# Optimization experiments

Measured on AMD Instinct MI355X. Metric: run time of the kernel, lower is better.

The kernel has to match this reference:

```python
import jax, jax.numpy as jnp
import numpy as np

N_NODES = 100000
N_EDGES = 1600000
F_IN, F_HID, F_OUT = 128, 128, 16
NEG_SLOPE = 0.2


def _glorot(key, shape):
    fan = sum(shape)
    return jax.random.uniform(key, shape, jnp.float32, -1.0, 1.0) * jnp.sqrt(6.0 / fan)


def setup_inputs() -> dict:
    key = jax.random.key(0)
    ks = jax.random.split(key, 16)
    x = jax.random.normal(ks[0], (N_NODES, F_IN), jnp.float32)
    edge_index = jax.random.randint(ks[1], (2, N_EDGES), 0, N_NODES, jnp.int64)
    d1, d2, d3 = F_HID, F_HID // 2, F_OUT
    return {
        'x': x,
        'edge_index': edge_index,
        'W1': _glorot(ks[2], (F_IN, d1)), 'a_src1': _glorot(ks[3], (d1,)), 'a_dst1': _glorot(ks[4], (d1,)), 'b1': jnp.zeros((d1,), jnp.float32),
        'W2': _glorot(ks[5], (d1, d2)), 'a_src2': _glorot(ks[6], (d2,)), 'a_dst2': _glorot(ks[7], (d2,)), 'b2': jnp.zeros((d2,), jnp.float32),
        'W3': _glorot(ks[8], (d2, d3)), 'a_src3': _glorot(ks[9], (d3,)), 'a_dst3': _glorot(ks[10], (d3,)), 'b3': jnp.zeros((d3,), jnp.float32),
    }


def gat_conv(x, src, dst, W, a_s, a_d, b):
    # x: [N, Fin] -> h: [N, Fout]; src/dst: [E] (self-loops included)
    h = x @ W
    e = jax.nn.leaky_relu(h @ a_s, NEG_SLOPE * 0 + NEG_SLOPE)  # placeholder avoided below
    # attention logits per edge: leaky_relu(alpha_src[src] + alpha_dst[dst])
    al_s = h @ a_s  # [N]
    al_d = h @ a_d  # [N]
    logits = jax.nn.leaky_relu(al_s[src] + al_d[dst], NEG_SLOPE)  # [E]
    # numerically stable softmax over incoming edges of each dst node
    m = jax.ops.segment_max(logits, dst, num_segments=N_NODES)
    m = jnp.where(jnp.isfinite(m), m, 0.0)
    ex = jnp.exp(logits - m[dst])
    denom = jax.ops.segment_sum(ex, dst, num_segments=N_NODES)
    alpha = ex / denom[dst]  # self-loops guarantee denom > 0
    out = jax.ops.segment_sum(alpha[:, None] * h[src], dst, num_segments=N_NODES)
    return out + b


def reference(x, edge_index, W1, a_src1, a_dst1, b1, W2, a_src2, a_dst2, b2, W3, a_src3, a_dst3, b3):
    loops = jnp.arange(N_NODES, dtype=edge_index.dtype)
    src = jnp.concatenate([edge_index[0], loops])
    dst = jnp.concatenate([edge_index[1], loops])
    h = gat_conv(x, src, dst, W1, a_src1, a_dst1, b1)
    h = jax.nn.relu(h)  # dropout p=0.5 is identity in eval mode
    h = gat_conv(h, src, dst, W2, a_src2, a_dst2, b2)
    h = jax.nn.relu(h)
    out = gat_conv(h, src, dst, W3, a_src3, a_dst3, b3)
    return out
```

## Files before the change

kernel.cpp:

```cpp
#include <hip/hip_runtime.h>
#include <hip/hip_bf16.h>

typedef __hip_bfloat16 bf16;
typedef __attribute__((ext_vector_type(8))) __bf16 bf16x8;
typedef __attribute__((ext_vector_type(4))) float f32x4;

static constexpr int N = 100000;
static constexpr int E = 1600000;
static constexpr int ETOT = E + N;
static constexpr float SLOPE = 0.2f;

__device__ __constant__ int c_poff[12] = {0, 16384, 16512, 16640,
                                          16768, 24960, 25024, 25088,
                                          25152, 26176, 26192, 26208};
static constexpr int PTOT = 26224;
static constexpr int H_POFF[12] = {0, 16384, 16512, 16640, 16768, 24960,
                                   25024, 25088, 25152, 26176, 26192, 26208};

struct Src12 { const void* p[12]; };

__device__ __forceinline__ float bfLo(unsigned u) { return __uint_as_float(u << 16); }
__device__ __forceinline__ float bfHi(unsigned u) { return __uint_as_float(u & 0xFFFF0000u); }

__device__ __forceinline__ void fma8(const uint4 r, float e, float* acc) {
  acc[0] = fmaf(e, bfLo(r.x), acc[0]);
  acc[1] = fmaf(e, bfHi(r.x), acc[1]);
  acc[2] = fmaf(e, bfLo(r.y), acc[2]);
  acc[3] = fmaf(e, bfHi(r.y), acc[3]);
  acc[4] = fmaf(e, bfLo(r.z), acc[4]);
  acc[5] = fmaf(e, bfHi(r.z), acc[5]);
  acc[6] = fmaf(e, bfLo(r.w), acc[6]);
  acc[7] = fmaf(e, bfHi(r.w), acc[7]);
}

__device__ __forceinline__ float edge_ex(float l) {
  l = (l > 0.f) ? l : SLOPE * l;
  return __expf(l);
}

__device__ __forceinline__ void loadEdge(const int* __restrict__ ei32,
                                         const long long* __restrict__ ei64,
                                         int use64, int t, int& s, int& d) {
  if (t >= E) { s = d = t - E; return; }
  if (use64) { s = (int)ei64[t]; d = (int)ei64[E + t]; }
  else       { s = ei32[t];      d = ei32[E + t]; }
}

__device__ __forceinline__ unsigned pk2(float a, float b) {
  bf16 x = __float2bfloat16(a), y = __float2bfloat16(b);
  unsigned short ux = *(unsigned short*)&x, uy = *(unsigned short*)&y;
  return ((unsigned)uy << 16) | ux;
}

static constexpr int CHUNK = 8192;
static constexpr int NCHK  = (ETOT + CHUNK - 1) / CHUNK;
static constexpr int NB1   = (N + 511) / 512;
static constexpr int M1    = NB1 * NCHK;
static constexpr int SBLK  = (M1 + 255) / 256;

__global__ __launch_bounds__(256) void detect_kernel(
    const unsigned long long* __restrict__ ei64,
    const unsigned short* __restrict__ w1u16, int* __restrict__ flags) {
  const int t = threadIdx.x;
  __shared__ unsigned long long bl[4];
  __shared__ unsigned long long sb64;
  const int w = t >> 6;
  bool p64 = (t < 64) && (ei64[t] >= (unsigned long long)N);
  unsigned long long b64 = __ballot(p64);
  if (t == 0) sb64 = b64;
  bool pf = (((w1u16[t] >> 7) & 0xFFu) >= 126u);
  unsigned long long bf_ = __ballot(pf);
  if ((t & 63) == 0) bl[w] = bf_;
  __syncthreads();
  if (t == 0) {
    flags[0] = (sb64 == 0ull) ? 1 : 0;
    flags[1] = ((bl[0] | bl[1] | bl[2] | bl[3]) != 0ull) ? 1 : 0;
  }
}

static constexpr int PB_PAR = (PTOT + 255) / 256;
static constexpr int PB_W1  = 128 * 128 / 256;
static constexpr int PB_W2  = 128 * 64 / 256;
static constexpr int PB_W3  = 64 * 16 / 256;
static constexpr int PB_TOT = NCHK + PB_PAR + PB_W1 + PB_W2 + PB_W3;

__device__ __forceinline__ void conv_w(const void* W, int kd, int dout, int f32,
                                       bf16* __restrict__ wt, int idx) {
  int n = idx / kd, k = idx - n * kd;
  float v = f32 ? ((const float*)W)[k * dout + n]
                : __bfloat162float(((const bf16*)W)[k * dout + n]);
  wt[idx] = __float2bfloat16(v);
}

__global__ __launch_bounds__(256) void prep_kernel(
    const int* __restrict__ ei32, const long long* __restrict__ ei64,
    const int* __restrict__ flags, int* __restrict__ c1,
    Src12 s, float* __restrict__ prm,
    bf16* __restrict__ w1t, bf16* __restrict__ w2t, bf16* __restrict__ w3t) {
  const int b = blockIdx.x, tid = threadIdx.x;
  const int f64 = flags[0], f32 = flags[1];
  if (b < NCHK) {
    __shared__ int h1[NB1];
    if (tid < NB1) h1[tid] = 0;
    __syncthreads();
    const int t0 = b * CHUNK;
#pragma unroll 4
    for (int i = tid; i < CHUNK; i += 256) {
      int t = t0 + i;
      if (t < ETOT) {
        int d = (t >= E) ? (t - E) : (f64 ? (int)ei64[E + t] : ei32[E + t]);
        atomicAdd(&h1[d >> 9], 1);
      }
    }
    __syncthreads();
    if (tid < NB1) c1[tid * NCHK + b] = h1[tid];
  } else if (b < NCHK + PB_PAR) {
    int t = (b - NCHK) * 256 + tid;
    if (t < PTOT) {
      int k = 0;
#pragma unroll
      for (int i = 1; i < 12; ++i)
        if (t >= c_poff[i]) k = i;
      int j = t - c_poff[k];
      prm[t] = f32 ? ((const float*)s.p[k])[j]
                   : __bfloat162float(((const bf16*)s.p[k])[j]);
    }
  } else if (b < NCHK + PB_PAR + PB_W1) {
    conv_w(s.p[0], 128, 128, f32, w1t, (b - NCHK - PB_PAR) * 256 + tid);
  } else if (b < NCHK + PB_PAR + PB_W1 + PB_W2) {
    conv_w(s.p[4], 128, 64, f32, w2t, (b - NCHK - PB_PAR - PB_W1) * 256 + tid);
  } else {
    conv_w(s.p[8], 64, 16, f32, w3t, (b - NCHK - PB_PAR - PB_W1 - PB_W2) * 256 + tid);
  }
}

__global__ __launch_bounds__(256) void scanA_kernel(const int* __restrict__ c1,
                                                    int* __restrict__ bsum) {
  __shared__ int red[256];
  const int t = threadIdx.x;
  const int i = blockIdx.x * 256 + t;
  red[t] = (i < M1) ? c1[i] : 0;
  __syncthreads();
#pragma unroll
  for (int off = 128; off > 0; off >>= 1) {
    if (t < off) red[t] += red[t + off];
    __syncthreads();
  }
  if (t == 0) bsum[blockIdx.x] = red[0];
}

__global__ __launch_bounds__(256) void scanB_kernel(const int* __restrict__ bsum,
                                                    int* __restrict__ boff) {
  __shared__ int s[256];
  const int t = threadIdx.x;
  const int v = (t < SBLK) ? bsum[t] : 0;
  s[t] = v;
  __syncthreads();
  for (int off = 1; off < 256; off <<= 1) {
    int u = (t >= off) ? s[t - off] : 0;
    __syncthreads();
    s[t] += u;
    __syncthreads();
  }
  if (t < SBLK) boff[t] = s[t] - v;
}

__global__ __launch_bounds__(256) void scanC_kernel(const int* __restrict__ c1,
                                                    const int* __restrict__ boff,
                                                    int* __restrict__ off1) {
  __shared__ int s[256];
  const int t = threadIdx.x;
  const int i = blockIdx.x * 256 + t;
  const int v = (i < M1) ? c1[i] : 0;
  s[t] = v;
  __syncthreads();
#pragma unroll
  for (int off = 1; off < 256; off <<= 1) {
    int u = (t >= off) ? s[t - off] : 0;
    __syncthreads();
    s[t] += u;
    __syncthreads();
  }
  if (i < M1) off1[i] = boff[blockIdx.x] + s[t] - v;
}

__device__ __forceinline__ void phaseC_body(int c, const int* __restrict__ ei32,
                                            const long long* __restrict__ ei64,
                                            int f64, const int* __restrict__ off1,
                                            int2* __restrict__ tmp) {
  __shared__ int cur[NB1];
  const int tid = threadIdx.x;
  if (tid < NB1) cur[tid] = off1[tid * NCHK + c];
  __syncthreads();
  const int t0 = c * CHUNK;
#pragma unroll 4
  for (int i = tid; i < CHUNK; i += 256) {
    int t = t0 + i;
    if (t < ETOT) {
      int s, d;
      loadEdge(ei32, ei64, f64, t, s, d);
      int pos = atomicAdd(&cur[d >> 9], 1);
      tmp[pos] = make_int2(d, s);
    }
  }
}

__global__ __launch_bounds__(256) void phaseD_kernel(const int* __restrict__ off1,
                                                     const int2* __restrict__ tmp,
                                                     int* __restrict__ rowptr,
                                                     int* __restrict__ ssrt) {
  __shared__ int h2[512], e2[512], cur[512];
  __shared__ int ps[256];
  const int b = blockIdx.x, t = threadIdx.x;
  const int base = off1[b * NCHK];
  const int end = (b + 1 < NB1) ? off1[(b + 1) * NCHK] : ETOT;
  const int len = end - base;
  h2[2 * t] = 0; h2[2 * t + 1] = 0;
  __syncthreads();
  for (int i = t; i < len; i += 256)
    atomicAdd(&h2[tmp[base + i].x & 511], 1);
  __syncthreads();
  const int s1 = h2[2 * t], s2 = h2[2 * t + 1];
  ps[t] = s1 + s2;
  __syncthreads();
  for (int off = 1; off < 256; off <<= 1) {
    int u = (t >= off) ? ps[t - off] : 0;
    __syncthreads();
    ps[t] += u;
    __syncthreads();
  }
  const int ep = ps[t] - (s1 + s2);
  e2[2 * t] = ep;
  e2[2 * t + 1] = ep + s1;
  cur[2 * t] = ep;
  cur[2 * t + 1] = ep + s1;
  __syncthreads();
#pragma unroll
  for (int k = 0; k < 2; ++k) {
    int f = 2 * t + k;
    int node = (b << 9) + f;
    if (node < N) rowptr[node] = base + e2[f];
  }
  if (b == 0 && t == 0) rowptr[N] = ETOT;
  for (int i = t; i < len; i += 256) {
    int2 e = tmp[base + i];
    int pos = base + atomicAdd(&cur[e.x & 511], 1);
    ssrt[pos] = e.y;
  }
}

template <int KD, int DOUT, bool XD>
__device__ __forceinline__ void gemm_body(int bb, const void* __restrict__ inv,
                                          const int* __restrict__ flags,
                                          const unsigned short* __restrict__ wt,
                                          bf16* __restrict__ h,
                                          const float* __restrict__ a_s,
                                          const float* __restrict__ a_d,
                                          float* __restrict__ als,
                                          float* __restrict__ ald) {
  constexpr int SA = KD + 8;
  constexpr int NT = DOUT / 16;
  constexpr int KS = KD / 32;
  __shared__ unsigned short sA[64 * SA];
  __shared__ unsigned short sB[DOUT * SA];
  const int tid = threadIdx.x;
  const int m0 = bb * 64;
  for (int idx = tid; idx < DOUT * KD / 8; idx += 256) {
    int n = idx / (KD / 8), k8 = idx - n * (KD / 8);
    *(uint4*)(sB + n * SA + k8 * 8) = *(const uint4*)(wt + n * KD + k8 * 8);
  }
  const bool f32 = XD ? (flags[1] != 0) : false;
  for (int idx = tid; idx < 64 * KD / 8; idx += 256) {
    int r = idx / (KD / 8), k8 = idx - r * (KD / 8);
    int m = m0 + r;
    uint4 v = make_uint4(0, 0, 0, 0);
    if (m < N) {
      if (XD && f32) {
        const float4 v0 = *((const float4*)inv + ((size_t)m * KD + k8 * 8) / 4);
        const float4 v1 = *((const float4*)inv + ((size_t)m * KD + k8 * 8) / 4 + 1);
        v = make_uint4(pk2(v0.x, v0.y), pk2(v0.z, v0.w),
                       pk2(v1.x, v1.y), pk2(v1.z, v1.w));
      } else {
        v = *((const uint4*)inv + ((size_t)m * KD + k8 * 8) / 8);
      }
    }
    *(uint4*)(sA + r * SA + k8 * 8) = v;
  }
  __syncthreads();
  const int lane = tid & 63;
  const int wv = tid >> 6;
  const int lr = lane & 15;
  const int q = lane >> 4;
  f32x4 acc[NT];
#pragma unroll
  for (int t = 0; t < NT; ++t)
#pragma unroll
    for (int r = 0; r < 4; ++r) acc[t][r] = 0.f;
  const int arow = wv * 16 + lr;
#pragma unroll
  for (int ks = 0; ks < KS; ++ks) {
    const int k0 = ks * 32 + q * 8;
    const bf16x8 a = *(const bf16x8*)(sA + arow * SA + k0);
#pragma unroll
    for (int t = 0; t < NT; ++t) {
      const bf16x8 b = *(const bf16x8*)(sB + (t * 16 + lr) * SA + k0);
      acc[t] = __builtin_amdgcn_mfma_f32_16x16x32_bf16(a, b, acc[t], 0, 0, 0);
    }
  }
  float ps[4] = {0.f, 0.f, 0.f, 0.f}, pd[4] = {0.f, 0.f, 0.f, 0.f};
#pragma unroll
  for (int t = 0; t < NT; ++t) {
    const float av = a_s[t * 16 + lr];
    const float dv = a_d[t * 16 + lr];
#pragma unroll
    for (int r = 0; r < 4; ++r) {
      ps[r] = fmaf(acc[t][r], av, ps[r]);
      pd[r] = fmaf(acc[t][r], dv, pd[r]);
    }
  }
#pragma unroll
  for (int m = 1; m < 16; m <<= 1)
#pragma unroll
    for (int r = 0; r < 4; ++r) {
      ps[r] += __shfl_xor(ps[r], m, 64);
      pd[r] += __shfl_xor(pd[r], m, 64);
    }
  const int mb = m0 + wv * 16 + q * 4;
  if (lr == 0) {
#pragma unroll
    for (int r = 0; r < 4; ++r) {
      int m = mb + r;
      if (m < N) { als[m] = ps[r]; ald[m] = pd[r]; }
    }
  }
#pragma unroll
  for (int t = 0; t < NT; ++t)
#pragma unroll
    for (int r = 0; r < 4; ++r) {
      int m = mb + r;
      if (m < N) h[(size_t)m * DOUT + t * 16 + lr] = __float2bfloat16(acc[t][r]);
    }
}

static constexpr int GB1 = (N + 63) / 64;

__global__ __launch_bounds__(256) void gemm1_phaseC(
    const void* __restrict__ x, const int* __restrict__ flags,
    const unsigned short* __restrict__ wt, bf16* __restrict__ h,
    const float* __restrict__ a_s, const float* __restrict__ a_d,
    float* __restrict__ als, float* __restrict__ ald,
    const int* __restrict__ ei32, const long long* __restrict__ ei64,
    const int* __restrict__ off1, int2* __restrict__ tmp) {
  if (blockIdx.x < GB1) {
    gemm_body<128, 128, true>(blockIdx.x, x, flags, wt, h, a_s, a_d, als, ald);
  } else {
    int c = blockIdx.x - GB1;
    if (c < NCHK) phaseC_body(c, ei32, ei64, flags[0], off1, tmp);
  }
}

static constexpr int AB = (N + 127) / 128;

template <int DA, int DOUT>
__global__ __launch_bounds__(512) void aggemm_kernel(
    const int* __restrict__ rowptr, const int* __restrict__ ssrt,
    const float* __restrict__ als_in, const float* __restrict__ ald_in,
    const unsigned short* __restrict__ hin, const float* __restrict__ bias,
    const unsigned short* __restrict__ wt, bf16* __restrict__ hout,
    const float* __restrict__ a_s, const float* __restrict__ a_d,
    float* __restrict__ als_out, float* __restrict__ ald_out) {
  constexpr int SA = DA + 8;
  constexpr int TPN = DA / 8;
  constexpr int NPR = 512 / TPN;
  constexpr int NR = 128 / NPR;
  constexpr int NT = DOUT / 16;
  constexpr int KS = DA / 32;
  __shared__ unsigned short sA[128 * SA];
  __shared__ unsigned short sB[DOUT * SA];
  const int tid = threadIdx.x;
  const int m0 = blockIdx.x * 128;
  for (int idx = tid; idx < DOUT * DA / 8; idx += 512) {
    int n = idx / (DA / 8), k8 = idx - n * (DA / 8);
    *(uint4*)(sB + n * SA + k8 * 8) = *(const uint4*)(wt + n * DA + k8 * 8);
  }
  const int sub = tid % TPN;
  const int rr0 = tid / TPN;
  const int col0 = sub * 8;
#pragma unroll
  for (int r = 0; r < NR; ++r) {
    const int row = r * NPR + rr0;
    const int d = m0 + row;
    if (d < N) {
      const int p0 = rowptr[d], p1 = rowptr[d + 1];
      const float ad = ald_in[d];
      float acc[8];
#pragma unroll
      for (int c = 0; c < 8; ++c) acc[c] = 0.f;
      float sum = 0.f;
      int p = p0;
      for (; p + 4 <= p1; p += 4) {
        const int s0 = ssrt[p + 0];
        const int s1 = ssrt[p + 1];
        const int s2 = ssrt[p + 2];
        const int s3 = ssrt[p + 3];
        const uint4 r0 = *reinterpret_cast<const uint4*>(hin + (size_t)s0 * DA + col0);
        const uint4 r1 = *reinterpret_cast<const uint4*>(hin + (size_t)s1 * DA + col0);
        const uint4 r2 = *reinterpret_cast<const uint4*>(hin + (size_t)s2 * DA + col0);
        const uint4 r3 = *reinterpret_cast<const uint4*>(hin + (size_t)s3 * DA + col0);
        const float x0 = edge_ex(als_in[s0] + ad);
        const float x1 = edge_ex(als_in[s1] + ad);
        const float x2 = edge_ex(als_in[s2] + ad);
        const float x3 = edge_ex(als_in[s3] + ad);
        sum += (x0 + x1) + (x2 + x3);
        fma8(r0, x0, acc);
        fma8(r1, x1, acc);
        fma8(r2, x2, acc);
        fma8(r3, x3, acc);
      }
      for (; p < p1; ++p) {
        const int s = ssrt[p];
        const uint4 rr = *reinterpret_cast<const uint4*>(hin + (size_t)s * DA + col0);
        const float x = edge_ex(als_in[s] + ad);
        sum += x;
        fma8(rr, x, acc);
      }
      const float inv = 1.f / sum;
      float v[8];
#pragma unroll
      for (int c = 0; c < 8; ++c) {
        float w = acc[c] * inv + bias[col0 + c];
        v[c] = (w > 0.f) ? w : 0.f;
      }
      uint4 pk = make_uint4(pk2(v[0], v[1]), pk2(v[2], v[3]),
                            pk2(v[4], v[5]), pk2(v[6], v[7]));
      *(uint4*)(sA + row * SA + col0) = pk;
    }
  }
  __syncthreads();
  const int lane = tid & 63;
  const int wv = tid >> 6;
  const int lr = lane & 15;
  const int q = lane >> 4;
  f32x4 acc[NT];
#pragma unroll
  for (int t = 0; t < NT; ++t)
#pragma unroll
    for (int r = 0; r < 4; ++r) acc[t][r] = 0.f;
  const int arow = wv * 16 + lr;
#pragma unroll
  for (int ks = 0; ks < KS; ++ks) {
    const int k0 = ks * 32 + q * 8;
    const bf16x8 a = *(const bf16x8*)(sA + arow * SA + k0);
#pragma unroll
    for (int t = 0; t < NT; ++t) {
      const bf16x8 b = *(const bf16x8*)(sB + (t * 16 + lr) * SA + k0);
      acc[t] = __builtin_amdgcn_mfma_f32_16x16x32_bf16(a, b, acc[t], 0, 0, 0);
    }
  }
  float ps[4] = {0.f, 0.f, 0.f, 0.f}, pd[4] = {0.f, 0.f, 0.f, 0.f};
#pragma unroll
  for (int t = 0; t < NT; ++t) {
    const float av = a_s[t * 16 + lr];
    const float dv = a_d[t * 16 + lr];
#pragma unroll
    for (int r = 0; r < 4; ++r) {
      ps[r] = fmaf(acc[t][r], av, ps[r]);
      pd[r] = fmaf(acc[t][r], dv, pd[r]);
    }
  }
#pragma unroll
  for (int m = 1; m < 16; m <<= 1)
#pragma unroll
    for (int r = 0; r < 4; ++r) {
      ps[r] += __shfl_xor(ps[r], m, 64);
      pd[r] += __shfl_xor(pd[r], m, 64);
    }
  const int mb = m0 + wv * 16 + q * 4;
  if (lr == 0) {
#pragma unroll
    for (int r = 0; r < 4; ++r) {
      int m = mb + r;
      if (m < N) { als_out[m] = ps[r]; ald_out[m] = pd[r]; }
    }
  }
#pragma unroll
  for (int t = 0; t < NT; ++t)
#pragma unroll
    for (int r = 0; r < 4; ++r) {
      int m = mb + r;
      if (m < N) hout[(size_t)m * DOUT + t * 16 + lr] = __float2bfloat16(acc[t][r]);
    }
}

template <int DOUT>
__global__ __launch_bounds__(256) void agg_final(const int* __restrict__ rowptr,
                                                 const int* __restrict__ ssrt,
                                                 const float* __restrict__ als,
                                                 const float* __restrict__ ald,
                                                 const unsigned short* __restrict__ hb,
                                                 const float* __restrict__ bias,
                                                 void* __restrict__ outv,
                                                 const int* __restrict__ flags) {
  constexpr int TPN = DOUT / 8;
  constexpr int NPB = 256 / TPN;
  const int sub = threadIdx.x % TPN;
  const int d = blockIdx.x * NPB + threadIdx.x / TPN;
  if (d >= N) return;
  const int p0 = rowptr[d], p1 = rowptr[d + 1];
  const float ad = ald[d];
  const int col0 = sub * 8;
  float acc[8];
#pragma unroll
  for (int c = 0; c < 8; ++c) acc[c] = 0.f;
  float sum = 0.f;
  int p = p0;
  for (; p + 4 <= p1; p += 4) {
    const int s0 = ssrt[p + 0];
    const int s1 = ssrt[p + 1];
    const int s2 = ssrt[p + 2];
    const int s3 = ssrt[p + 3];
    const uint4 r0 = *reinterpret_cast<const uint4*>(hb + (size_t)s0 * DOUT + col0);
    const uint4 r1 = *reinterpret_cast<const uint4*>(hb + (size_t)s1 * DOUT + col0);
    const uint4 r2 = *reinterpret_cast<const uint4*>(hb + (size_t)s2 * DOUT + col0);
    const uint4 r3 = *reinterpret_cast<const uint4*>(hb + (size_t)s3 * DOUT + col0);
    const float x0 = edge_ex(als[s0] + ad);
    const float x1 = edge_ex(als[s1] + ad);
    const float x2 = edge_ex(als[s2] + ad);
    const float x3 = edge_ex(als[s3] + ad);
    sum += (x0 + x1) + (x2 + x3);
    fma8(r0, x0, acc);
    fma8(r1, x1, acc);
    fma8(r2, x2, acc);
    fma8(r3, x3, acc);
  }
  for (; p < p1; ++p) {
    const int s = ssrt[p];
    const uint4 r = *reinterpret_cast<const uint4*>(hb + (size_t)s * DOUT + col0);
    const float x = edge_ex(als[s] + ad);
    sum += x;
    fma8(r, x, acc);
  }
  const float inv = 1.f / sum;
  const bool f32o = flags[1] != 0;
#pragma unroll
  for (int c = 0; c < 8; ++c) {
    float v = acc[c] * inv + bias[col0 + c];
    if (f32o) ((float*)outv)[(size_t)d * DOUT + col0 + c] = v;
    else      ((bf16*)outv)[(size_t)d * DOUT + col0 + c] = __float2bfloat16(v);
  }
}

static inline size_t rup(size_t v) { return (v + 255) & ~(size_t)255; }

extern "C" void kernel_launch(void* const* d_in, const int* in_sizes, int n_in,
                              void* d_out, int out_size, void* d_ws, size_t ws_size,
                              hipStream_t stream) {
  const int* ei32 = (const int*)d_in[1];
  const long long* ei64 = (const long long*)d_in[1];

  char* p = (char*)d_ws;
  int*   flags  = (int*)p;   p += 256;
  float* prm    = (float*)p; p += rup((size_t)PTOT * 4);
  bf16*  w1t    = (bf16*)p;  p += rup((size_t)128 * 128 * 2);
  bf16*  w2t    = (bf16*)p;  p += rup((size_t)128 * 64 * 2);
  bf16*  w3t    = (bf16*)p;  p += rup((size_t)64 * 16 * 2);
  float* als1   = (float*)p; p += rup((size_t)N * 4);
  float* ald1   = (float*)p; p += rup((size_t)N * 4);
  float* als2   = (float*)p; p += rup((size_t)N * 4);
  float* ald2   = (float*)p; p += rup((size_t)N * 4);
  float* als3   = (float*)p; p += rup((size_t)N * 4);
  float* ald3   = (float*)p; p += rup((size_t)N * 4);
  int*   rowptr = (int*)p;   p += rup((size_t)(N + 1) * 4);
  int*   c1     = (int*)p;   p += rup((size_t)M1 * 4);
  int*   off1   = (int*)p;   p += rup((size_t)M1 * 4);
  int*   bsum   = (int*)p;   p += rup((size_t)SBLK * 4);
  int*   boff   = (int*)p;   p += rup((size_t)SBLK * 4);
  int2*  tmp    = (int2*)p;  p += rup((size_t)ETOT * 8);
  int*   ssrt   = (int*)p;   p += rup((size_t)ETOT * 4);
  bf16*  h1     = (bf16*)p;  p += rup((size_t)N * 128 * 2);
  bf16*  h2     = (bf16*)p;  p += rup((size_t)N * 64 * 2);
  bf16*  h3     = (bf16*)p;

  Src12 s;
  for (int i = 0; i < 12; ++i) s.p[i] = d_in[2 + i];

  detect_kernel<<<1, 256, 0, stream>>>(
      (const unsigned long long*)d_in[1], (const unsigned short*)d_in[2], flags);
  prep_kernel<<<PB_TOT, 256, 0, stream>>>(ei32, ei64, flags, c1, s, prm, w1t, w2t, w3t);
  scanA_kernel<<<SBLK, 256, 0, stream>>>(c1, bsum);
  scanB_kernel<<<1, 256, 0, stream>>>(bsum, boff);
  scanC_kernel<<<SBLK, 256, 0, stream>>>(c1, boff, off1);

  const float *as1 = prm + H_POFF[1], *ad1 = prm + H_POFF[2], *b1 = prm + H_POFF[3];
  const float *as2 = prm + H_POFF[5], *ad2 = prm + H_POFF[6], *b2 = prm + H_POFF[7];
  const float *as3 = prm + H_POFF[9], *ad3 = prm + H_POFF[10], *b3 = prm + H_POFF[11];

  gemm1_phaseC<<<GB1 + NCHK, 256, 0, stream>>>(
      d_in[0], flags, (const unsigned short*)w1t, h1, as1, ad1, als1, ald1,
      ei32, ei64, off1, tmp);
  phaseD_kernel<<<NB1, 256, 0, stream>>>(off1, tmp, rowptr, ssrt);
  aggemm_kernel<128, 64><<<AB, 512, 0, stream>>>(
      rowptr, ssrt, als1, ald1, (const unsigned short*)h1, b1,
      (const unsigned short*)w2t, h2, as2, ad2, als2, ald2);
  aggemm_kernel<64, 16><<<AB, 512, 0, stream>>>(
      rowptr, ssrt, als2, ald2, (const unsigned short*)h2, b2,
      (const unsigned short*)w3t, h3, as3, ad3, als3, ald3);
  agg_final<16><<<(N + 127) / 128, 256, 0, stream>>>(
      rowptr, ssrt, als3, ald3, (const unsigned short*)h3, b3, d_out, flags);
}
```

Measured before the change: 343.9 us.

## Precompute layer-1 edge attention weights in CSR build and read W from global

The CSR scatter kernel now computes the exponentiated attention weight for each layer-1 edge, since both endpoint scores are already available there. It stores these weights in a new per-edge array aligned with the sorted source list, so the first aggregation kernel reads them sequentially instead of gathering als per edge and recomputing the exponential. Separately, the aggregation+GEMM kernel no longer stages the weight matrix in shared memory and loads MFMA B operands straight from global memory. This saves LDS and a sync-phase copy, but adds an extra per-edge array write and read and uncoalesced global loads for W.

Result: no change. 345.2 us (+0.4%).

```diff
diff --git a/kernel.cpp b/kernel.cpp
--- a/kernel.cpp
+++ b/kernel.cpp
@@ -208,7 +208,10 @@
 __global__ __launch_bounds__(256) void phaseD_kernel(const int* __restrict__ off1,
                                                      const int2* __restrict__ tmp,
                                                      int* __restrict__ rowptr,
-                                                     int* __restrict__ ssrt) {
+                                                     int* __restrict__ ssrt,
+                                                     const float* __restrict__ als1,
+                                                     const float* __restrict__ ald1,
+                                                     float* __restrict__ exf) {
   __shared__ int h2[512], e2[512], cur[512];
   __shared__ int ps[256];
   const int b = blockIdx.x, t = threadIdx.x;
@@ -246,6 +249,7 @@
     int2 e = tmp[base + i];
     int pos = base + atomicAdd(&cur[e.x & 511], 1);
     ssrt[pos] = e.y;
+    exf[pos] = edge_ex(als1[e.y] + ald1[e.x]);
   }
 }
 
@@ -361,9 +365,10 @@
 
 static constexpr int AB = (N + 127) / 128;
 
-template <int DA, int DOUT>
+template <int DA, int DOUT, bool EXF>
 __global__ __launch_bounds__(512) void aggemm_kernel(
     const int* __restrict__ rowptr, const int* __restrict__ ssrt,
+    const float* __restrict__ exf,
     const float* __restrict__ als_in, const float* __restrict__ ald_in,
     const unsigned short* __restrict__ hin, const float* __restrict__ bias,
     const unsigned short* __restrict__ wt, bf16* __restrict__ hout,
@@ -376,13 +381,8 @@
   constexpr int NT = DOUT / 16;
   constexpr int KS = DA / 32;
   __shared__ unsigned short sA[128 * SA];
-  __shared__ unsigned short sB[DOUT * SA];
   const int tid = threadIdx.x;
   const int m0 = blockIdx.x * 128;
-  for (int idx = tid; idx < DOUT * DA / 8; idx += 512) {
-    int n = idx / (DA / 8), k8 = idx - n * (DA / 8);
-    *(uint4*)(sB + n * SA + k8 * 8) = *(const uint4*)(wt + n * DA + k8 * 8);
-  }
   const int sub = tid % TPN;
   const int rr0 = tid / TPN;
   const int col0 = sub * 8;
@@ -392,7 +392,7 @@
     const int d = m0 + row;
     if (d < N) {
       const int p0 = rowptr[d], p1 = rowptr[d + 1];
-      const float ad = ald_in[d];
+      const float ad = EXF ? 0.f : ald_in[d];
       float acc[8];
 #pragma unroll
       for (int c = 0; c < 8; ++c) acc[c] = 0.f;
@@ -407,10 +407,10 @@
         const uint4 r1 = *reinterpret_cast<const uint4*>(hin + (size_t)s1 * DA + col0);
         const uint4 r2 = *reinterpret_cast<const uint4*>(hin + (size_t)s2 * DA + col0);
         const uint4 r3 = *reinterpret_cast<const uint4*>(hin + (size_t)s3 * DA + col0);
-        const float x0 = edge_ex(als_in[s0] + ad);
-        const float x1 = edge_ex(als_in[s1] + ad);
-        const float x2 = edge_ex(als_in[s2] + ad);
-        const float x3 = edge_ex(als_in[s3] + ad);
+        const float x0 = EXF ? exf[p + 0] : edge_ex(als_in[s0] + ad);
+        const float x1 = EXF ? exf[p + 1] : edge_ex(als_in[s1] + ad);
+        const float x2 = EXF ? exf[p + 2] : edge_ex(als_in[s2] + ad);
+        const float x3 = EXF ? exf[p + 3] : edge_ex(als_in[s3] + ad);
         sum += (x0 + x1) + (x2 + x3);
         fma8(r0, x0, acc);
         fma8(r1, x1, acc);
@@ -420,7 +420,7 @@
       for (; p < p1; ++p) {
         const int s = ssrt[p];
         const uint4 rr = *reinterpret_cast<const uint4*>(hin + (size_t)s * DA + col0);
-        const float x = edge_ex(als_in[s] + ad);
+        const float x = EXF ? exf[p] : edge_ex(als_in[s] + ad);
         sum += x;
         fma8(rr, x, acc);
       }
@@ -453,7 +453,7 @@
     const bf16x8 a = *(const bf16x8*)(sA + arow * SA + k0);
 #pragma unroll
     for (int t = 0; t < NT; ++t) {
-      const bf16x8 b = *(const bf16x8*)(sB + (t * 16 + lr) * SA + k0);
+      const bf16x8 b = *(const bf16x8*)(wt + (t * 16 + lr) * DA + k0);
       acc[t] = __builtin_amdgcn_mfma_f32_16x16x32_bf16(a, b, acc[t], 0, 0, 0);
     }
   }
@@ -577,6 +577,7 @@
   int*   boff   = (int*)p;   p += rup((size_t)SBLK * 4);
   int2*  tmp    = (int2*)p;  p += rup((size_t)ETOT * 8);
   int*   ssrt   = (int*)p;   p += rup((size_t)ETOT * 4);
+  float* exf    = (float*)p; p += rup((size_t)ETOT * 4);
   bf16*  h1     = (bf16*)p;  p += rup((size_t)N * 128 * 2);
   bf16*  h2     = (bf16*)p;  p += rup((size_t)N * 64 * 2);
   bf16*  h3     = (bf16*)p;
@@ -598,12 +599,12 @@
   gemm1_phaseC<<<GB1 + NCHK, 256, 0, stream>>>(
       d_in[0], flags, (const unsigned short*)w1t, h1, as1, ad1, als1, ald1,
       ei32, ei64, off1, tmp);
-  phaseD_kernel<<<NB1, 256, 0, stream>>>(off1, tmp, rowptr, ssrt);
-  aggemm_kernel<128, 64><<<AB, 512, 0, stream>>>(
-      rowptr, ssrt, als1, ald1, (const unsigned short*)h1, b1,
+  phaseD_kernel<<<NB1, 256, 0, stream>>>(off1, tmp, rowptr, ssrt, als1, ald1, exf);
+  aggemm_kernel<128, 64, true><<<AB, 512, 0, stream>>>(
+      rowptr, ssrt, exf, als1, ald1, (const unsigned short*)h1, b1,
       (const unsigned short*)w2t, h2, as2, ad2, als2, ald2);
-  aggemm_kernel<64, 16><<<AB, 512, 0, stream>>>(
-      rowptr, ssrt, als2, ald2, (const unsigned short*)h2, b2,
+  aggemm_kernel<64, 16, false><<<AB, 512, 0, stream>>>(
+      rowptr, ssrt, nullptr, als2, ald2, (const unsigned short*)h2, b2,
       (const unsigned short*)w3t, h3, as3, ad3, als3, ald3);
   agg_final<16><<<(N + 127) / 128, 256, 0, stream>>>(
       rowptr, ssrt, als3, ald3, (const unsigned short*)h3, b3, d_out, flags);
```
